# Kernel tuning notes

Measured on AMD Instinct MI355X. Metric: run time of the kernel, lower is better.

## Reference

```python
import jax, jax.numpy as jnp
import numpy as np

N_PER_G = 100  # nodes per graph


def setup_inputs() -> dict:
    key = jax.random.key(0)
    ks = jax.random.split(key, 12)
    N, G, E = 100000, 1000, 1600000
    ninp, nout, K, H, H2 = 3, 10, 5, 64, 32
    x = jax.random.normal(ks[0], (N, ninp), jnp.float32)
    # within-graph random edges (contiguous node blocks per graph)
    epg = E // G
    gid = jnp.arange(E, dtype=jnp.int32) // epg
    src = jax.random.randint(ks[1], (E,), 0, N_PER_G, jnp.int32) + gid * N_PER_G
    dst = jax.random.randint(ks[2], (E,), 0, N_PER_G, jnp.int32) + gid * N_PER_G
    edge_index = jnp.stack([src, dst])
    batch = (jnp.arange(N, dtype=jnp.int32) // N_PER_G)
    lambda_max = 1.5 + 0.5 * jax.random.uniform(ks[3], (G,), jnp.float32)
    s = 0.05
    W1 = jax.random.normal(ks[4], (K, ninp, H), jnp.float32) * s
    b1 = jnp.zeros((H,), jnp.float32)
    W2 = jax.random.normal(ks[5], (K, H, H), jnp.float32) * s
    b2 = jnp.zeros((H,), jnp.float32)
    W3 = jax.random.normal(ks[6], (K, H, H), jnp.float32) * s
    b3 = jnp.zeros((H,), jnp.float32)
    bn_gamma = jnp.ones((H,), jnp.float32)
    bn_beta = jnp.zeros((H,), jnp.float32)
    bn_mean = jnp.zeros((H,), jnp.float32)
    bn_var = jnp.ones((H,), jnp.float32)
    fc1_w = jax.random.normal(ks[7], (H, H2), jnp.float32) * s
    fc1_b = jnp.zeros((H2,), jnp.float32)
    fc2_w = jax.random.normal(ks[8], (H2, nout), jnp.float32) * s
    fc2_b = jnp.zeros((nout,), jnp.float32)
    return dict(x=x, edge_index=edge_index, batch=batch, lambda_max=lambda_max,
                W1=W1, b1=b1, W2=W2, b2=b2, W3=W3, b3=b3,
                bn_gamma=bn_gamma, bn_beta=bn_beta, bn_mean=bn_mean, bn_var=bn_var,
                fc1_w=fc1_w, fc1_b=fc1_b, fc2_w=fc2_w, fc2_b=fc2_b)


def _cheb_conv(x, W, b, row, col, coef_edge, coef_loop):
    # PyG ChebConv with sym-normalized scaled Laplacian:
    # Lhat x = scatter_add(coef_edge * x[col] -> row) + coef_loop * x
    N = x.shape[0]
    def lhat(h):
        return jax.ops.segment_sum(coef_edge[:, None] * h[col], row,
                                   num_segments=N) + coef_loop[:, None] * h
    Tx0 = x
    out = Tx0 @ W[0]
    Tx1 = lhat(x)
    out = out + Tx1 @ W[1]
    for k in range(2, W.shape[0]):
        Tx2 = 2.0 * lhat(Tx1) - Tx0
        out = out + Tx2 @ W[k]
        Tx0, Tx1 = Tx1, Tx2
    return out + b


def reference(x, edge_index, batch, lambda_max,
              W1, b1, W2, b2, W3, b3,
              bn_gamma, bn_beta, bn_mean, bn_var,
              fc1_w, fc1_b, fc2_w, fc2_b):
    N = x.shape[0]
    G = lambda_max.shape[0]
    row, col = edge_index[0], edge_index[1]
    # sym Laplacian normalization, scaled by 2/lambda_max (per-graph)
    deg = jax.ops.segment_sum(jnp.ones_like(row, dtype=x.dtype), row, num_segments=N)
    dis = jnp.where(deg > 0, deg, 1.0) ** -0.5
    dis = jnp.where(deg > 0, dis, 0.0)
    lmax_e = lambda_max[batch[row]]
    coef_edge = -(2.0 / lmax_e) * dis[row] * dis[col]   # off-diagonal of Lhat
    coef_loop = 2.0 / lambda_max[batch] - 1.0           # diagonal of Lhat
    h = jax.nn.relu(_cheb_conv(x, W1, b1, row, col, coef_edge, coef_loop))
    h = jax.nn.relu(_cheb_conv(h, W2, b2, row, col, coef_edge, coef_loop))
    h = jax.nn.relu(_cheb_conv(h, W3, b3, row, col, coef_edge, coef_loop))
    # global mean pool over graphs
    sums = jax.ops.segment_sum(h, batch, num_segments=G)
    cnts = jax.ops.segment_sum(jnp.ones((N,), h.dtype), batch, num_segments=G)
    g = sums / jnp.maximum(cnts, 1.0)[:, None]
    # BatchNorm1d (eval mode, running stats), eps=1e-5
    g = (g - bn_mean) * jax.lax.rsqrt(bn_var + 1e-5) * bn_gamma + bn_beta
    g = jax.nn.relu(g @ fc1_w + fc1_b)
    return jax.nn.log_softmax(g @ fc2_w + fc2_b, axis=1)
```

## Files before the change

kernel.cpp:

```cpp
#include <hip/hip_runtime.h>

#define NPG 100
#define HF 64
#define NROW 128
#define SA 120
#define ST 72

typedef float  f4   __attribute__((ext_vector_type(4)));
typedef float  f16v __attribute__((ext_vector_type(16)));
typedef short  bf8  __attribute__((ext_vector_type(8)));

#define SZ_ARM (NROW * SA * 2)
#define SZ_TRM (NROW * ST * 2)
#define OFF_ARM 0
#define OFF_P   SZ_ARM
#define OFF_Q   (OFF_P + SZ_TRM)
#define OFF_AF  OFF_P
#define OFF_MISC 70720
#define SMEM_BYTES (OFF_MISC + 1792)

#define WT_TOTAL 46080

__device__ __forceinline__ unsigned short f2bf(float f) {
    unsigned u = __float_as_uint(f);
    u += 0x7fffu + ((u >> 16) & 1u);
    return (unsigned short)(u >> 16);
}
__device__ __forceinline__ float bf2f(unsigned short h) {
    return __uint_as_float(((unsigned)h) << 16);
}
__device__ __forceinline__ f16v zerov16() {
    f16v z;
    #pragma unroll
    for (int i = 0; i < 16; i++) z[i] = 0.f;
    return z;
}

__global__ void wconv(const float* __restrict__ W1, const float* __restrict__ W2,
                      const float* __restrict__ W3, unsigned short* __restrict__ ws)
{
    int idx = blockIdx.x * 256 + threadIdx.x;
    if (idx >= WT_TOTAL) return;
    float v;
    if (idx < 5120) {
        int k5 = idx >> 10, rem = idx & 1023, fo = rem >> 4, fi = rem & 15;
        v = (fi < 3) ? W1[(k5 * 3 + fi) * HF + fo] : 0.f;
    } else if (idx < 25600) {
        int j = idx - 5120;
        int k5 = j >> 12, rem = j & 4095, fo = rem >> 6, fi = rem & 63;
        v = W2[(k5 * HF + fi) * HF + fo];
    } else {
        int j = idx - 25600;
        int k5 = j >> 12, rem = j & 4095, fo = rem >> 6, fi = rem & 63;
        v = W3[(k5 * HF + fi) * HF + fo];
    }
    ws[idx] = f2bf(v);
}

__launch_bounds__(256, 2)
__global__ void cheb32(const float* __restrict__ x, const int* __restrict__ ei,
                       const float* __restrict__ lambda_max,
                       const unsigned short* __restrict__ Wt,
                       const float* __restrict__ b1, const float* __restrict__ b2,
                       const float* __restrict__ b3,
                       const float* __restrict__ bng, const float* __restrict__ bnb,
                       const float* __restrict__ bnm, const float* __restrict__ bnv,
                       const float* __restrict__ fc1w, const float* __restrict__ fc1b,
                       const float* __restrict__ fc2w, const float* __restrict__ fc2b,
                       float* __restrict__ out, int E_total, int epg)
{
    extern __shared__ char sm[];
    const int tid = threadIdx.x;
    const int g = blockIdx.x;
    const int ebase = g * epg, nbase = g * NPG;
    const int wg = tid >> 6, lane = tid & 63;
    const int l31 = lane & 31, hh = lane >> 5;
    const int Ntf = wg & 1;
    const int Mt0 = (wg >> 1) * 2;
    const int fo = Ntf * 32 + l31;

    float* Af     = (float*)(sm + OFF_AF);
    int*   deg    = (int*)(sm + OFF_MISC);
    float* dis    = (float*)(sm + OFF_MISC + 512);
    float* pool   = (float*)(sm + OFF_MISC + 1024);
    float* gvn    = (float*)(sm + OFF_MISC + 1280);
    float* zf     = (float*)(sm + OFF_MISC + 1536);
    float* logits = (float*)(sm + OFF_MISC + 1664);
    float* lsep   = (float*)(sm + OFF_MISC + 1728);

    const float lam = lambda_max[g];
    const float two_l = 2.0f / lam;
    const float cl = two_l - 1.0f;

    for (int i = tid; i < 2500; i += 256) ((f4*)Af)[i] = (f4){0.f, 0.f, 0.f, 0.f};
    if (tid < NPG) deg[tid] = 0;
    if (tid < HF) pool[tid] = 0.f;
    __syncthreads();
    for (int e = tid; e < epg; e += 256)
        atomicAdd(&deg[ei[ebase + e] - nbase], 1);
    __syncthreads();
    if (tid < NPG) dis[tid] = deg[tid] > 0 ? rsqrtf((float)deg[tid]) : 0.f;
    __syncthreads();
    for (int e = tid; e < epg; e += 256) {
        int r = ei[ebase + e] - nbase;
        int c = ei[E_total + ebase + e] - nbase;
        atomicAdd(&Af[r * NPG + c], -two_l * dis[r] * dis[c]);
    }
    __syncthreads();
    if (tid < NPG) Af[tid * NPG + tid] += cl;
    __syncthreads();
    for (int u = tid; u < NROW * 56; u += 256) {
        int n = u / 56, p = (u % 56) * 2;
        float v0 = (n < NPG && p     < NPG) ? Af[n * NPG + p]     : 0.f;
        float v1 = (n < NPG && p + 1 < NPG) ? Af[n * NPG + p + 1] : 0.f;
        *(unsigned*)(sm + OFF_ARM + (n * SA + p) * 2) =
            (unsigned)f2bf(v0) | ((unsigned)f2bf(v1) << 16);
    }
    __syncthreads();

    for (int i = tid; i < SZ_TRM / 16; i += 256)
        ((f4*)(sm + OFF_P))[i] = (f4){0.f, 0.f, 0.f, 0.f};
    __syncthreads();
    if (tid < NPG) {
        unsigned short h0 = f2bf(x[(nbase + tid) * 3 + 0]);
        unsigned short h1 = f2bf(x[(nbase + tid) * 3 + 1]);
        unsigned short h2 = f2bf(x[(nbase + tid) * 3 + 2]);
        *(unsigned*)(sm + OFF_P + (tid * ST) * 2) = (unsigned)h0 | ((unsigned)h1 << 16);
        *(unsigned short*)(sm + OFF_P + (tid * ST + 2) * 2) = h2;
    }
    __syncthreads();

    f16v acc[2];
    const float* bsv[3] = {b1, b2, b3};

    for (int L = 0; L < 3; L++) {
        const bool l1 = (L == 0);
        const unsigned short* Wl = l1 ? Wt : (Wt + (L == 1 ? 5120 : 25600));
        acc[0] = zerov16();
        acc[1] = zerov16();

        auto TW = [&](int offSrc, int k5) {
            const int nKs = l1 ? 1 : 4;
            for (int Ks = 0; Ks < nKs; Ks++) {
                bf8 bw;
                if (l1) bw = *(const bf8*)(Wl + (k5 * 64 + fo) * 16 + 8 * hh);
                else    bw = *(const bf8*)(Wl + (k5 * 64 + fo) * 64 + Ks * 16 + 8 * hh);
                #pragma unroll
                for (int m = 0; m < 2; m++) {
                    bf8 a = *(const bf8*)(sm + offSrc +
                              (((Mt0 + m) * 32 + l31) * ST + Ks * 16 + 8 * hh) * 2);
                    acc[m] = __builtin_amdgcn_mfma_f32_32x32x16_bf16(a, bw, acc[m], 0, 0, 0);
                }
            }
        };

        auto LHAT = [&](int offSrc, int offDst, int s) {
            bf8 bfr[7];
            #pragma unroll
            for (int Ks = 0; Ks < 7; Ks++) {
                #pragma unroll
                for (int j = 0; j < 8; j++) {
                    int k = Ks * 16 + 8 * hh + j;
                    bfr[Ks][j] = *(const short*)(sm + offSrc + (k * ST + fo) * 2);
                }
            }
            #pragma unroll
            for (int m = 0; m < 2; m++) {
                f16v c = zerov16();
                #pragma unroll
                for (int Ks = 0; Ks < 7; Ks++) {
                    bf8 a = *(const bf8*)(sm + OFF_ARM +
                              (((Mt0 + m) * 32 + l31) * SA + Ks * 16 + 8 * hh) * 2);
                    c = __builtin_amdgcn_mfma_f32_32x32x16_bf16(a, bfr[Ks], c, 0, 0, 0);
                }
                #pragma unroll
                for (int r = 0; r < 16; r++) {
                    int n = (Mt0 + m) * 32 + (r & 3) + 8 * (r >> 2) + 4 * hh;
                    char* p = sm + offDst + (n * ST + fo) * 2;
                    float v = c[r];
                    if (s >= 2) v = 2.f * v - bf2f(*(const unsigned short*)p);
                    *(unsigned short*)p = f2bf(v);
                }
            }
        };

        TW(OFF_P, 0);
        LHAT(OFF_P, OFF_Q, 1);  __syncthreads();
        TW(OFF_Q, 1);
        LHAT(OFF_Q, OFF_P, 2);  __syncthreads();
        TW(OFF_P, 2);
        LHAT(OFF_P, OFF_Q, 3);  __syncthreads();
        TW(OFF_Q, 3);
        LHAT(OFF_Q, OFF_P, 4);  __syncthreads();
        TW(OFF_P, 4);
        __syncthreads();

        const float bias = bsv[L][fo];
        if (L < 2) {
            #pragma unroll
            for (int m = 0; m < 2; m++) {
                #pragma unroll
                for (int r = 0; r < 16; r++) {
                    float h = fmaxf(acc[m][r] + bias, 0.f);
                    int n = (Mt0 + m) * 32 + (r & 3) + 8 * (r >> 2) + 4 * hh;
                    *(unsigned short*)(sm + OFF_P + (n * ST + fo) * 2) = f2bf(h);
                }
            }
            __syncthreads();
        } else {
            float ssum = 0.f;
            #pragma unroll
            for (int m = 0; m < 2; m++) {
                #pragma unroll
                for (int r = 0; r < 16; r++) {
                    int n = (Mt0 + m) * 32 + (r & 3) + 8 * (r >> 2) + 4 * hh;
                    float h = fmaxf(acc[m][r] + bias, 0.f);
                    if (n < NPG) ssum += h;
                }
            }
            ssum += __shfl_xor(ssum, 32, 64);
            if (hh == 0) atomicAdd(&pool[fo], ssum);
            __syncthreads();
        }
    }

    if (tid < HF) {
        float gv = pool[tid] * (1.0f / NPG);
        gv = (gv - bnm[tid]) * rsqrtf(bnv[tid] + 1e-5f) * bng[tid] + bnb[tid];
        gvn[tid] = gv;
    }
    __syncthreads();
    if (tid < 32) {
        float a = fc1b[tid];
        for (int f = 0; f < HF; f++) a += gvn[f] * fc1w[f * 32 + tid];
        zf[tid] = fmaxf(a, 0.f);
    }
    __syncthreads();
    if (tid < 10) {
        float a = fc2b[tid];
        for (int k = 0; k < 32; k++) a += zf[k] * fc2w[k * 10 + tid];
        logits[tid] = a;
    }
    __syncthreads();
    if (tid == 0) {
        float m = logits[0];
        for (int i = 1; i < 10; i++) m = fmaxf(m, logits[i]);
        float s = 0.f;
        for (int i = 0; i < 10; i++) s += expf(logits[i] - m);
        lsep[0] = m + logf(s);
    }
    __syncthreads();
    if (tid < 10) out[g * 10 + tid] = logits[tid] - lsep[0];
}

extern "C" void kernel_launch(void* const* d_in, const int* in_sizes, int n_in,
                              void* d_out, int out_size, void* d_ws, size_t ws_size,
                              hipStream_t stream) {
    const float* x    = (const float*)d_in[0];
    const int*   ei   = (const int*)d_in[1];
    const float* lmax = (const float*)d_in[3];
    const float* W1   = (const float*)d_in[4];
    const float* b1   = (const float*)d_in[5];
    const float* W2   = (const float*)d_in[6];
    const float* b2   = (const float*)d_in[7];
    const float* W3   = (const float*)d_in[8];
    const float* b3   = (const float*)d_in[9];
    const float* bng  = (const float*)d_in[10];
    const float* bnb  = (const float*)d_in[11];
    const float* bnm  = (const float*)d_in[12];
    const float* bnv  = (const float*)d_in[13];
    const float* fc1w = (const float*)d_in[14];
    const float* fc1b = (const float*)d_in[15];
    const float* fc2w = (const float*)d_in[16];
    const float* fc2b = (const float*)d_in[17];

    const int E = in_sizes[1] / 2;
    const int G = in_sizes[3];
    const int epg = E / G;

    unsigned short* Wt = (unsigned short*)d_ws;

    wconv<<<(WT_TOTAL + 255) / 256, 256, 0, stream>>>(W1, W2, W3, Wt);

    hipFuncSetAttribute((const void*)cheb32,
                        hipFuncAttributeMaxDynamicSharedMemorySize, SMEM_BYTES);

    cheb32<<<G, 256, SMEM_BYTES, stream>>>(x, ei, lmax, Wt, b1, b2, b3,
                                           bng, bnb, bnm, bnv, fc1w, fc1b, fc2w, fc2b,
                                           (float*)d_out, E, epg);
}
```

Baseline: 180.8 us.

## Keep transposed Chebyshev term in LDS and carry previous term in registers

Adds a feature-major (transposed) copy of the current Chebyshev term in shared memory. The Lhat product can then load its operand as contiguous 8-element vectors instead of 56 scalar strided short loads per lane. The computation is reformulated as (T^T)·(A^T) with A rows as the B operand. The previous and older terms are kept in registers, which removes the read-modify-write of the old term from LDS. It costs extra LDS space, extra scalar transposed stores, more register pressure and an extra barrier per step.

```diff
diff --git a/kernel.cpp b/kernel.cpp
--- a/kernel.cpp
+++ b/kernel.cpp
@@ -5,6 +5,7 @@
 #define NROW 128
 #define SA 120
 #define ST 72
+#define SAT 136
 
 typedef float  f4   __attribute__((ext_vector_type(4)));
 typedef float  f16v __attribute__((ext_vector_type(16)));
@@ -12,10 +13,11 @@
 
 #define SZ_ARM (NROW * SA * 2)
 #define SZ_TRM (NROW * ST * 2)
+#define SZ_TT  (HF * SAT * 2)
 #define OFF_ARM 0
-#define OFF_P   SZ_ARM
-#define OFF_Q   (OFF_P + SZ_TRM)
-#define OFF_AF  OFF_P
+#define OFF_TRM SZ_ARM
+#define OFF_TT  (OFF_TRM + SZ_TRM)
+#define OFF_AF  OFF_TRM
 #define OFF_MISC 70720
 #define SMEM_BYTES (OFF_MISC + 1792)
 
@@ -58,16 +60,16 @@
 }
 
 __launch_bounds__(256, 2)
-__global__ void cheb32(const float* __restrict__ x, const int* __restrict__ ei,
-                       const float* __restrict__ lambda_max,
-                       const unsigned short* __restrict__ Wt,
-                       const float* __restrict__ b1, const float* __restrict__ b2,
-                       const float* __restrict__ b3,
-                       const float* __restrict__ bng, const float* __restrict__ bnb,
-                       const float* __restrict__ bnm, const float* __restrict__ bnv,
-                       const float* __restrict__ fc1w, const float* __restrict__ fc1b,
-                       const float* __restrict__ fc2w, const float* __restrict__ fc2b,
-                       float* __restrict__ out, int E_total, int epg)
+__global__ void cheb32t(const float* __restrict__ x, const int* __restrict__ ei,
+                        const float* __restrict__ lambda_max,
+                        const unsigned short* __restrict__ Wt,
+                        const float* __restrict__ b1, const float* __restrict__ b2,
+                        const float* __restrict__ b3,
+                        const float* __restrict__ bng, const float* __restrict__ bnb,
+                        const float* __restrict__ bnm, const float* __restrict__ bnv,
+                        const float* __restrict__ fc1w, const float* __restrict__ fc1b,
+                        const float* __restrict__ fc2w, const float* __restrict__ fc2b,
+                        float* __restrict__ out, int E_total, int epg)
 {
     extern __shared__ char sm[];
     const int tid = threadIdx.x;
@@ -75,9 +77,9 @@
     const int ebase = g * epg, nbase = g * NPG;
     const int wg = tid >> 6, lane = tid & 63;
     const int l31 = lane & 31, hh = lane >> 5;
-    const int Ntf = wg & 1;
+    const int ht  = wg & 1;
     const int Mt0 = (wg >> 1) * 2;
-    const int fo = Ntf * 32 + l31;
+    const int fo  = ht * 32 + l31;
 
     float* Af     = (float*)(sm + OFF_AF);
     int*   deg    = (int*)(sm + OFF_MISC);
@@ -118,19 +120,23 @@
     }
     __syncthreads();
 
-    for (int i = tid; i < SZ_TRM / 16; i += 256)
-        ((f4*)(sm + OFF_P))[i] = (f4){0.f, 0.f, 0.f, 0.f};
+    for (int i = tid; i < (SZ_TRM + SZ_TT) / 16; i += 256)
+        ((f4*)(sm + OFF_TRM))[i] = (f4){0.f, 0.f, 0.f, 0.f};
     __syncthreads();
     if (tid < NPG) {
         unsigned short h0 = f2bf(x[(nbase + tid) * 3 + 0]);
         unsigned short h1 = f2bf(x[(nbase + tid) * 3 + 1]);
         unsigned short h2 = f2bf(x[(nbase + tid) * 3 + 2]);
-        *(unsigned*)(sm + OFF_P + (tid * ST) * 2) = (unsigned)h0 | ((unsigned)h1 << 16);
-        *(unsigned short*)(sm + OFF_P + (tid * ST + 2) * 2) = h2;
+        *(unsigned*)(sm + OFF_TRM + (tid * ST) * 2) = (unsigned)h0 | ((unsigned)h1 << 16);
+        *(unsigned short*)(sm + OFF_TRM + (tid * ST + 2) * 2) = h2;
+        *(unsigned short*)(sm + OFF_TT + (0 * SAT + tid) * 2) = h0;
+        *(unsigned short*)(sm + OFF_TT + (1 * SAT + tid) * 2) = h1;
+        *(unsigned short*)(sm + OFF_TT + (2 * SAT + tid) * 2) = h2;
     }
     __syncthreads();
 
     f16v acc[2];
+    unsigned prev[2][8], oldr[2][8];
     const float* bsv[3] = {b1, b2, b3};
 
     for (int L = 0; L < 3; L++) {
@@ -139,7 +145,19 @@
         acc[0] = zerov16();
         acc[1] = zerov16();
 
-        auto TW = [&](int offSrc, int k5) {
+        #pragma unroll
+        for (int m = 0; m < 2; m++) {
+            int np = (Mt0 + m) * 32 + l31;
+            #pragma unroll
+            for (int q4 = 0; q4 < 4; q4++) {
+                int fb = 8 * q4 + 4 * hh + 32 * ht;
+                uint2 u = *(const uint2*)(sm + OFF_TRM + (np * ST + fb) * 2);
+                prev[m][2 * q4] = u.x;
+                prev[m][2 * q4 + 1] = u.y;
+            }
+        }
+
+        auto TW = [&](int k5) {
             const int nKs = l1 ? 1 : 4;
             for (int Ks = 0; Ks < nKs; Ks++) {
                 bf8 bw;
@@ -147,63 +165,83 @@
                 else    bw = *(const bf8*)(Wl + (k5 * 64 + fo) * 64 + Ks * 16 + 8 * hh);
                 #pragma unroll
                 for (int m = 0; m < 2; m++) {
-                    bf8 a = *(const bf8*)(sm + offSrc +
+                    bf8 a = *(const bf8*)(sm + OFF_TRM +
                               (((Mt0 + m) * 32 + l31) * ST + Ks * 16 + 8 * hh) * 2);
                     acc[m] = __builtin_amdgcn_mfma_f32_32x32x16_bf16(a, bw, acc[m], 0, 0, 0);
                 }
             }
         };
 
-        auto LHAT = [&](int offSrc, int offDst, int s) {
-            bf8 bfr[7];
-            #pragma unroll
-            for (int Ks = 0; Ks < 7; Ks++) {
-                #pragma unroll
-                for (int j = 0; j < 8; j++) {
-                    int k = Ks * 16 + 8 * hh + j;
-                    bfr[Ks][j] = *(const short*)(sm + offSrc + (k * ST + fo) * 2);
-                }
-            }
+        TW(0);
+        for (int s = 1; s <= 4; s++) {
+            bf8 af[7];
+            #pragma unroll
+            for (int Ks = 0; Ks < 7; Ks++)
+                af[Ks] = *(const bf8*)(sm + OFF_TT +
+                           ((32 * ht + l31) * SAT + Ks * 16 + 8 * hh) * 2);
+            __syncthreads();
             #pragma unroll
             for (int m = 0; m < 2; m++) {
+                int np = (Mt0 + m) * 32 + l31;
                 f16v c = zerov16();
                 #pragma unroll
                 for (int Ks = 0; Ks < 7; Ks++) {
-                    bf8 a = *(const bf8*)(sm + OFF_ARM +
-                              (((Mt0 + m) * 32 + l31) * SA + Ks * 16 + 8 * hh) * 2);
-                    c = __builtin_amdgcn_mfma_f32_32x32x16_bf16(a, bfr[Ks], c, 0, 0, 0);
-                }
+                    bf8 b = *(const bf8*)(sm + OFF_ARM + (np * SA + Ks * 16 + 8 * hh) * 2);
+                    c = __builtin_amdgcn_mfma_f32_32x32x16_bf16(af[Ks], b, c, 0, 0, 0);
+                }
+                unsigned short h[16];
                 #pragma unroll
                 for (int r = 0; r < 16; r++) {
-                    int n = (Mt0 + m) * 32 + (r & 3) + 8 * (r >> 2) + 4 * hh;
-                    char* p = sm + offDst + (n * ST + fo) * 2;
                     float v = c[r];
-                    if (s >= 2) v = 2.f * v - bf2f(*(const unsigned short*)p);
-                    *(unsigned short*)p = f2bf(v);
-                }
-            }
-        };
-
-        TW(OFF_P, 0);
-        LHAT(OFF_P, OFF_Q, 1);  __syncthreads();
-        TW(OFF_Q, 1);
-        LHAT(OFF_Q, OFF_P, 2);  __syncthreads();
-        TW(OFF_P, 2);
-        LHAT(OFF_P, OFF_Q, 3);  __syncthreads();
-        TW(OFF_Q, 3);
-        LHAT(OFF_Q, OFF_P, 4);  __syncthreads();
-        TW(OFF_P, 4);
+                    if (s >= 2) {
+                        unsigned short o = (unsigned short)
+                            ((oldr[m][r >> 1] >> (16 * (r & 1))) & 0xffff);
+                        v = 2.f * v - bf2f(o);
+                    }
+                    h[r] = f2bf(v);
+                }
+                #pragma unroll
+                for (int p = 0; p < 8; p++) {
+                    oldr[m][p] = prev[m][p];
+                    prev[m][p] = (unsigned)h[2 * p] | ((unsigned)h[2 * p + 1] << 16);
+                }
+                #pragma unroll
+                for (int r = 0; r < 16; r++) {
+                    int f = (r & 3) + 8 * (r >> 2) + 4 * hh + 32 * ht;
+                    *(unsigned short*)(sm + OFF_TT + (f * SAT + np) * 2) = h[r];
+                }
+                #pragma unroll
+                for (int q4 = 0; q4 < 4; q4++) {
+                    int fb = 8 * q4 + 4 * hh + 32 * ht;
+                    uint2 pk;
+                    pk.x = prev[m][2 * q4];
+                    pk.y = prev[m][2 * q4 + 1];
+                    *(uint2*)(sm + OFF_TRM + (np * ST + fb) * 2) = pk;
+                }
+            }
+            __syncthreads();
+            TW(s);
+        }
         __syncthreads();
 
         const float bias = bsv[L][fo];
         if (L < 2) {
             #pragma unroll
             for (int m = 0; m < 2; m++) {
+                unsigned short h[16];
                 #pragma unroll
                 for (int r = 0; r < 16; r++) {
-                    float h = fmaxf(acc[m][r] + bias, 0.f);
+                    h[r] = f2bf(fmaxf(acc[m][r] + bias, 0.f));
                     int n = (Mt0 + m) * 32 + (r & 3) + 8 * (r >> 2) + 4 * hh;
-                    *(unsigned short*)(sm + OFF_P + (n * ST + fo) * 2) = f2bf(h);
+                    *(unsigned short*)(sm + OFF_TRM + (n * ST + fo) * 2) = h[r];
+                }
+                #pragma unroll
+                for (int q4 = 0; q4 < 4; q4++) {
+                    int nb = (Mt0 + m) * 32 + 8 * q4 + 4 * hh;
+                    uint2 pk;
+                    pk.x = (unsigned)h[4 * q4] | ((unsigned)h[4 * q4 + 1] << 16);
+                    pk.y = (unsigned)h[4 * q4 + 2] | ((unsigned)h[4 * q4 + 3] << 16);
+                    *(uint2*)(sm + OFF_TT + (fo * SAT + nb) * 2) = pk;
                 }
             }
             __syncthreads();
@@ -282,10 +320,10 @@
 
     wconv<<<(WT_TOTAL + 255) / 256, 256, 0, stream>>>(W1, W2, W3, Wt);
 
-    hipFuncSetAttribute((const void*)cheb32,
+    hipFuncSetAttribute((const void*)cheb32t,
                         hipFuncAttributeMaxDynamicSharedMemorySize, SMEM_BYTES);
 
-    cheb32<<<G, 256, SMEM_BYTES, stream>>>(x, ei, lmax, Wt, b1, b2, b3,
-                                           bng, bnb, bnm, bnv, fc1w, fc1b, fc2w, fc2b,
-                                           (float*)d_out, E, epg);
-}
+    cheb32t<<<G, 256, SMEM_BYTES, stream>>>(x, ei, lmax, Wt, b1, b2, b3,
+                                            bng, bnb, bnm, bnv, fc1w, fc1b, fc2w, fc2b,
+                                            (float*)d_out, E, epg);
+}
```

New measurement: 183.0 us. Within noise of the previous version (+1.2%).
